# Optimization experiments

Hardware: AMD Instinct MI355X
Metric: run time of the kernel (lower is better)

Reference implementation:

```python
import jax, jax.numpy as jnp
import numpy as np

# ---- constants mirroring tinyRSNN __init__ ----
DT = 0.004
THRESHOLD = 1.0
SOFTPLUS_1 = float(np.log1p(np.e))  # softplus(1.0) = 1.3132617
TAU_SYN_H = SOFTPLUS_1 * 0.01
TAU_MEM_H = SOFTPLUS_1 * 0.02
TAU_SYN_O = SOFTPLUS_1 * 0.01
TAU_MEM_O = SOFTPLUS_1 * 0.02

T, B, IN, H, OUT = 4096, 128, 96, 64, 2


def setup_inputs() -> dict:
    key = jax.random.key(0)
    k0, k1, k2, k3 = jax.random.split(key, 4)
    x = jax.random.normal(k0, (T, B, IN), dtype=jnp.float32)
    W_h = jax.random.normal(k1, (H, IN), dtype=jnp.float32) / np.sqrt(IN)
    V = jax.random.normal(k2, (H, H), dtype=jnp.float32) / np.sqrt(H)
    W_o = jax.random.normal(k3, (OUT, H), dtype=jnp.float32) / np.sqrt(H)
    return {"x": x, "W_h": W_h, "V": V, "W_o": W_o}


def _spike(u):
    # forward: Heaviside(u); surrogate gradient handled in fwdbwd module
    return (u > 0).astype(u.dtype)


def reference(x, W_h, V, W_o):
    # exponential decay factors (stork-like synaptic/membrane dynamics)
    alpha_h = jnp.exp(-DT / TAU_SYN_H)
    beta_h = jnp.exp(-DT / TAU_MEM_H)
    alpha_o = jnp.exp(-DT / TAU_SYN_O)
    beta_o = jnp.exp(-DT / TAU_MEM_O)

    def step(carry, x_t):
        prev_inp, spk, syn, mem, syn_o, mem_o = carry
        # NOTE: module feeds the PREVIOUS input and PREVIOUS hidden spikes
        cur_h = prev_inp @ W_h.T                       # [B,H]
        syn = alpha_h * syn + cur_h + spk @ V.T        # synaptic current
        mem = beta_h * mem + (1.0 - beta_h) * syn      # membrane integration
        new_spk = _spike(mem - THRESHOLD)              # threshold at 1
        mem = mem * (1.0 - new_spk)                    # reset_mechanism='zero'
        # readout LIF (reset_mechanism='none'), driven by previous spikes
        syn_o = alpha_o * syn_o + spk @ W_o.T
        mem_o = beta_o * mem_o + (1.0 - beta_o) * syn_o
        return (x_t, new_spk, syn, mem, syn_o, mem_o), mem_o

    z = lambda *s: jnp.zeros(s, dtype=x.dtype)
    init = (z(B, IN), z(B, H), z(B, H), z(B, H), z(B, OUT), z(B, OUT))
    _, preds = jax.lax.scan(step, init, x)             # preds: [T,B,OUT]
    return preds
```

## Files before the change

### kernel.cpp

```cpp
#include <hip/hip_runtime.h>
#include <cmath>

#define T_STEPS 4096
#define BATCH   128
#define NIN     96
#define NH      64

typedef unsigned short u16;

__device__ __forceinline__ float bf2f(u16 u) {
    unsigned v = ((unsigned)u) << 16;
    return __builtin_bit_cast(float, v);
}
__device__ __forceinline__ double d_alpha() { return exp(-0.004 / (log1p(exp(1.0)) * 0.01)); }
__device__ __forceinline__ double d_beta()  { return exp(-0.004 / (log1p(exp(1.0)) * 0.02)); }

__device__ __forceinline__ int sniff_part(const void* p, int nscan, int tid, int nthr) {
    const u16* q = (const u16*)p;
    int cnt = 0;
    for (int i = tid; i < nscan; i += nthr) {
        float v = bf2f(q[i]);
        if (!(fabsf(v) < 1e4f)) cnt++;
    }
    return cnt;
}
__device__ __forceinline__ int wave_sum(int c) {
#pragma unroll
    for (int d = 32; d >= 1; d >>= 1) c += __shfl_xor(c, d, 64);
    return c;
}

__device__ __forceinline__ void acc_chunk(float* __restrict__ acc,
                                          const float* __restrict__ xr,
                                          const float* __restrict__ wbase) {
#pragma unroll
    for (int h = 0; h < 64; ++h) {
        const float4* wr = (const float4*)(wbase + h * NIN);
        const float4 w0 = wr[0], w1 = wr[1], w2 = wr[2], w3 = wr[3];
        float c = acc[h];
        c = fmaf(xr[0],  w0.x, c); c = fmaf(xr[1],  w0.y, c);
        c = fmaf(xr[2],  w0.z, c); c = fmaf(xr[3],  w0.w, c);
        c = fmaf(xr[4],  w1.x, c); c = fmaf(xr[5],  w1.y, c);
        c = fmaf(xr[6],  w1.z, c); c = fmaf(xr[7],  w1.w, c);
        c = fmaf(xr[8],  w2.x, c); c = fmaf(xr[9],  w2.y, c);
        c = fmaf(xr[10], w2.z, c); c = fmaf(xr[11], w2.w, c);
        c = fmaf(xr[12], w3.x, c); c = fmaf(xr[13], w3.y, c);
        c = fmaf(xr[14], w3.z, c); c = fmaf(xr[15], w3.w, c);
        acc[h] = c;
    }
}

__global__ __launch_bounds__(256) void k_cur(const void* __restrict__ xv,
                                             const void* __restrict__ whv,
                                             float* __restrict__ cur) {
    const int NROWC = (T_STEPS - 1) * BATCH;
    const int tid = threadIdx.x;
    __shared__ int s_cnt[2];
    __shared__ __align__(16) float whs[NH * NIN];
    if (tid < 2) s_cnt[tid] = 0;
    __syncthreads();
    int c0 = sniff_part(xv, 512, tid, 256);
    int c1 = sniff_part(whv, 512, tid, 256);
    if (c0) atomicAdd(&s_cnt[0], c0);
    if (c1) atomicAdd(&s_cnt[1], c1);
    __syncthreads();
    const bool fx = s_cnt[0] >= 32, fw = s_cnt[1] >= 32;

    if (fw) {
        const float* w = (const float*)whv;
        for (int s = tid; s < NH * NIN; s += 256) whs[s] = w[s];
    } else {
        const u16* w = (const u16*)whv;
        for (int s = tid; s < NH * NIN; s += 256) whs[s] = bf2f(w[s]);
    }
    __syncthreads();

    const long r = (long)blockIdx.x * 256 + tid;
    if (r >= NROWC) {
        const long z = r - NROWC;
        if (z < BATCH) {
            float4 zero = {0.f, 0.f, 0.f, 0.f};
            float4* zp = (float4*)(cur + z * NH);
#pragma unroll
            for (int j = 0; j < 16; ++j) zp[j] = zero;
        }
        return;
    }

    float acc[64];
#pragma unroll
    for (int h = 0; h < 64; ++h) acc[h] = 0.f;

    if (!fx) {
        const uint4* xq = (const uint4*)((const u16*)xv + (size_t)r * NIN);
        uint4 n0 = xq[0], n1 = xq[1];
#pragma unroll 1
        for (int kb = 0; kb < 6; ++kb) {
            const uint4 a = n0, b = n1;
            if (kb < 5) { n0 = xq[(kb + 1) * 2]; n1 = xq[(kb + 1) * 2 + 1]; }
            const unsigned ua[8] = {a.x, a.y, a.z, a.w, b.x, b.y, b.z, b.w};
            float xr[16];
#pragma unroll
            for (int j = 0; j < 8; ++j) {
                xr[2 * j]     = bf2f((u16)(ua[j] & 0xFFFFu));
                xr[2 * j + 1] = bf2f((u16)(ua[j] >> 16));
            }
            acc_chunk(acc, xr, whs + kb * 16);
        }
    } else {
        const float4* xq = (const float4*)((const float*)xv + (size_t)r * NIN);
        float4 n0 = xq[0], n1 = xq[1], n2 = xq[2], n3 = xq[3];
#pragma unroll 1
        for (int kb = 0; kb < 6; ++kb) {
            const float4 a0 = n0, a1 = n1, a2 = n2, a3 = n3;
            if (kb < 5) {
                n0 = xq[(kb + 1) * 4];     n1 = xq[(kb + 1) * 4 + 1];
                n2 = xq[(kb + 1) * 4 + 2]; n3 = xq[(kb + 1) * 4 + 3];
            }
            const float xr[16] = {a0.x, a0.y, a0.z, a0.w, a1.x, a1.y, a1.z, a1.w,
                                  a2.x, a2.y, a2.z, a2.w, a3.x, a3.y, a3.z, a3.w};
            acc_chunk(acc, xr, whs + kb * 16);
        }
    }

    float4* op = (float4*)(cur + ((size_t)r + BATCH) * NH);
#pragma unroll
    for (int j = 0; j < 16; ++j) {
        float4 v;
        v.x = acc[4 * j]; v.y = acc[4 * j + 1]; v.z = acc[4 * j + 2]; v.w = acc[4 * j + 3];
        op[j] = v;
    }
}

__global__ __launch_bounds__(64, 1) void k_scan(const float* __restrict__ cur,
                                                const void* __restrict__ vv,
                                                _Float16* __restrict__ ftr) {
    const int b = blockIdx.x, h = threadIdx.x;
    const double alpha = d_alpha(), beta = d_beta(), ombeta = 1.0 - beta;
    const float alphaf = (float)alpha, betaf = (float)beta, ombetaf = (float)ombeta;

    const bool fv = wave_sum(sniff_part(vv, 512, h, 64)) >= 32;

    __shared__ float vlds[65 * NH];
    if (fv) {
        const float* vp = (const float*)vv;
        for (int s = h; s < NH * NH; s += 64) vlds[((s & 63) << 6) | (s >> 6)] = vp[s];
    } else {
        const u16* vp = (const u16*)vv;
        for (int s = h; s < NH * NH; s += 64) vlds[((s & 63) << 6) | (s >> 6)] = bf2f(vp[s]);
    }
    vlds[(64 << 6) | h] = 0.0f;
    __syncthreads();

    double syn = 0.0, mem = 0.0;
    float e = 0.f, f = 0.f, spkf = 0.f;

    const size_t STEP = (size_t)BATCH * NH;
    const float* cp = cur + (size_t)b * NH + h;
    _Float16* fp = ftr + (size_t)b * NH + h;

    float cbuf[8];
#pragma unroll
    for (int j = 0; j < 8; ++j) cbuf[j] = cp[(size_t)j * STEP];

    float r0 = 0.f, r1 = 0.f;
    unsigned long long mt = 0ull;
    double p = ombeta * fma(alpha, syn, (double)cbuf[0]);
    double q = 1.0 - beta * mem;

    for (int tt = 0; tt < T_STEPS; tt += 8) {
#pragma unroll
        for (int j = 0; j < 8; ++j) {
            const int t = tt + j;
            const float c = cbuf[j];
            cbuf[j] = cp[(size_t)(t + 8) * STEP];

            double rec = (double)r0 + (double)r1;
            while (mt) {
                const int k = (int)__builtin_ctzll(mt);
                mt &= mt - 1;
                rec += (double)vlds[(k << 6) | h];
            }

            const bool s = fma(ombeta, rec, p) > q;
            const unsigned long long mask = __ballot(s);

            {
                unsigned long long m = mask;
                const int k0 = m ? (int)__builtin_ctzll(m) : 64;
                m = m ? (m & (m - 1)) : 0ull;
                const int k1 = m ? (int)__builtin_ctzll(m) : 64;
                mt = m ? (m & (m - 1)) : 0ull;
                r0 = vlds[(k0 << 6) | h];
                r1 = vlds[(k1 << 6) | h];
            }
            __builtin_amdgcn_sched_barrier(0);

            syn = alpha * syn + ((double)c + rec);
            mem = beta * mem + ombeta * syn;

            e = fmaf(alphaf, e, spkf);
            f = fmaf(betaf, f, ombetaf * e);
            fp[(size_t)t * STEP] = (_Float16)f;

            mem = s ? 0.0 : mem;
            spkf = s ? 1.0f : 0.0f;

            const float cn = cbuf[(j + 1) & 7];
            p = ombeta * fma(alpha, syn, (double)cn);
            q = 1.0 - beta * mem;
        }
    }
}

__global__ __launch_bounds__(256) void k_out(const _Float16* __restrict__ ftr,
                                             const void* __restrict__ wov,
                                             float* __restrict__ out) {
    const int tid = threadIdx.x;
    __shared__ unsigned tile[256 * 34];
    __shared__ float wo[2][64];
    const bool fo = sniff_part(wov, 120, 0, 1) >= 7;
    if (fo) {
        if (tid < 128) wo[tid >> 6][tid & 63] = ((const float*)wov)[tid];
    } else {
        if (tid < 128) wo[tid >> 6][tid & 63] = bf2f(((const u16*)wov)[tid]);
    }

    const unsigned* src = (const unsigned*)(ftr + (size_t)blockIdx.x * 256 * NH);
#pragma unroll
    for (int i = 0; i < 32; ++i) {
        const int s = i * 256 + tid;
        tile[(s >> 5) * 34 + (s & 31)] = src[s];
    }
    __syncthreads();

    const size_t idx = (size_t)blockIdx.x * 256 + tid;
    const unsigned* up = &tile[tid * 34];
    float d0 = 0.f, d1 = 0.f;
#pragma unroll
    for (int j = 0; j < 32; ++j) {
        const unsigned u = up[j];
        const float f0 = (float)__builtin_bit_cast(_Float16, (unsigned short)(u & 0xFFFFu));
        const float f1 = (float)__builtin_bit_cast(_Float16, (unsigned short)(u >> 16));
        d0 = fmaf(f0, wo[0][2 * j], d0);
        d1 = fmaf(f0, wo[1][2 * j], d1);
        d0 = fmaf(f1, wo[0][2 * j + 1], d0);
        d1 = fmaf(f1, wo[1][2 * j + 1], d1);
    }
    float2 r; r.x = d0; r.y = d1;
    ((float2*)out)[idx] = r;
}

__global__ __launch_bounds__(64) void k_fused(const void* __restrict__ xv,
                                              const void* __restrict__ whv,
                                              const void* __restrict__ vv,
                                              const void* __restrict__ wov,
                                              float* __restrict__ out) {
    const int b = blockIdx.x, h = threadIdx.x;
    const double alpha = d_alpha(), beta = d_beta(), ombeta = 1.0 - beta;

    const bool fx = wave_sum(sniff_part(xv, 512, h, 64)) >= 32;
    const bool fw = wave_sum(sniff_part(whv, 512, h, 64)) >= 32;
    const bool fv = wave_sum(sniff_part(vv, 512, h, 64)) >= 32;
    const bool fo = wave_sum(sniff_part(wov, 120, h, 64)) >= 7;

    __shared__ float vlds[NH * NH];
    __shared__ float whl[NIN * NH];
    if (fv) { const float* vp = (const float*)vv;
        for (int s = h; s < NH * NH; s += 64) vlds[((s & 63) << 6) | (s >> 6)] = vp[s]; }
    else    { const u16* vp = (const u16*)vv;
        for (int s = h; s < NH * NH; s += 64) vlds[((s & 63) << 6) | (s >> 6)] = bf2f(vp[s]); }
    if (fw) { const float* wp = (const float*)whv;
        for (int s = h; s < NH * NIN; s += 64) whl[(s % 96) * 64 + (s / 96)] = wp[s]; }
    else    { const u16* wp = (const u16*)whv;
        for (int s = h; s < NH * NIN; s += 64) whl[(s % 96) * 64 + (s / 96)] = bf2f(wp[s]); }
    __syncthreads();

    double wo0, wo1;
    if (fo) { wo0 = (double)((const float*)wov)[h]; wo1 = (double)((const float*)wov)[64 + h]; }
    else    { wo0 = (double)bf2f(((const u16*)wov)[h]); wo1 = (double)bf2f(((const u16*)wov)[64 + h]); }

    double syn = 0.0, mem = 0.0, syno0 = 0.0, memo0 = 0.0, syno1 = 0.0, memo1 = 0.0;
    double spkd = 0.0;
    unsigned long long mask = 0ull;

    for (int t = 0; t < T_STEPS; ++t) {
        float c = 0.0f;
        if (t > 0) {
            const size_t off = ((size_t)(t - 1) * BATCH + b) * NIN;
            if (fx) { const float* xp = (const float*)xv + off;
                for (int i = 0; i < NIN; ++i) c = fmaf(xp[i], whl[i * 64 + h], c); }
            else    { const u16* xp = (const u16*)xv + off;
                for (int i = 0; i < NIN; ++i) c = fmaf(bf2f(xp[i]), whl[i * 64 + h], c); }
        }
        double rec = 0.0;
        unsigned long long m = mask;
        while (m) { const int k = __builtin_ctzll(m); m &= m - 1; rec += (double)vlds[(k << 6) | h]; }

        syn = alpha * syn + ((double)c + rec);
        mem = beta * mem + ombeta * syn;

        double p0 = spkd * wo0, p1 = spkd * wo1;
#pragma unroll
        for (int d = 32; d >= 1; d >>= 1) { p0 += __shfl_xor(p0, d, 64); p1 += __shfl_xor(p1, d, 64); }
        syno0 = alpha * syno0 + p0;
        memo0 = beta * memo0 + ombeta * syno0;
        syno1 = alpha * syno1 + p1;
        memo1 = beta * memo1 + ombeta * syno1;
        if (h == 0) {
            const size_t w = ((size_t)t * BATCH + b) * 2;
            out[w] = (float)memo0;
            out[w + 1] = (float)memo1;
        }

        const bool s = mem > 1.0;
        mem = s ? 0.0 : mem;
        spkd = s ? 1.0 : 0.0;
        mask = __ballot(s);
    }
}

extern "C" void kernel_launch(void* const* d_in, const int* in_sizes, int n_in,
                              void* d_out, int out_size, void* d_ws, size_t ws_size,
                              hipStream_t stream) {
    (void)in_sizes; (void)out_size;
    if (n_in < 4) return;
    const void* x  = d_in[0];
    const void* Wh = d_in[1];
    const void* V  = d_in[2];
    const void* Wo = d_in[3];
    float* out = (float*)d_out;

    const size_t NROW = (size_t)T_STEPS * BATCH;
    const size_t curB = NROW * NH * sizeof(float);
    const size_t ftrB = NROW * NH * sizeof(_Float16);

    if (ws_size >= curB + ftrB) {
        float* cur = (float*)d_ws;
        _Float16* ftr = (_Float16*)((char*)d_ws + curB);
        const int NBLK = (int)(NROW / 256);
        k_cur<<<NBLK, 256, 0, stream>>>(x, Wh, cur);
        k_scan<<<BATCH, 64, 0, stream>>>(cur, V, ftr);
        k_out<<<NROW / 256, 256, 0, stream>>>(ftr, Wo, out);
    } else {
        k_fused<<<BATCH, 64, 0, stream>>>(x, Wh, V, Wo, out);
    }
}
```

Before: 924.5 us.

## Retile input projection kernel as 4x16 register tiles with transposed LDS weights

The input-projection kernel now gives each thread 4 rows × 16 hidden units instead of 1 row × 64 units. Weights are stored transposed in LDS so the 16 consecutive h values can be read as float4s at each k. This is meant to reuse every loaded weight across 4 rows and every x value across 16 outputs, cutting LDS reads per FMA. It also makes all lanes of a wave read the same weights (broadcast). The cost is that each thread's x loads now stride across 4 rows, and k_cur is likely a small share of total time next to the sequential scan kernel.

```diff
diff --git a/kernel.cpp b/kernel.cpp
--- a/kernel.cpp
+++ b/kernel.cpp
@@ -30,33 +30,15 @@
     return c;
 }
 
-__device__ __forceinline__ void acc_chunk(float* __restrict__ acc,
-                                          const float* __restrict__ xr,
-                                          const float* __restrict__ wbase) {
-#pragma unroll
-    for (int h = 0; h < 64; ++h) {
-        const float4* wr = (const float4*)(wbase + h * NIN);
-        const float4 w0 = wr[0], w1 = wr[1], w2 = wr[2], w3 = wr[3];
-        float c = acc[h];
-        c = fmaf(xr[0],  w0.x, c); c = fmaf(xr[1],  w0.y, c);
-        c = fmaf(xr[2],  w0.z, c); c = fmaf(xr[3],  w0.w, c);
-        c = fmaf(xr[4],  w1.x, c); c = fmaf(xr[5],  w1.y, c);
-        c = fmaf(xr[6],  w1.z, c); c = fmaf(xr[7],  w1.w, c);
-        c = fmaf(xr[8],  w2.x, c); c = fmaf(xr[9],  w2.y, c);
-        c = fmaf(xr[10], w2.z, c); c = fmaf(xr[11], w2.w, c);
-        c = fmaf(xr[12], w3.x, c); c = fmaf(xr[13], w3.y, c);
-        c = fmaf(xr[14], w3.z, c); c = fmaf(xr[15], w3.w, c);
-        acc[h] = c;
-    }
-}
-
 __global__ __launch_bounds__(256) void k_cur(const void* __restrict__ xv,
                                              const void* __restrict__ whv,
                                              float* __restrict__ cur) {
     const int NROWC = (T_STEPS - 1) * BATCH;
     const int tid = threadIdx.x;
+    const int lane = tid & 63;
+    const int hg = tid >> 6;
     __shared__ int s_cnt[2];
-    __shared__ __align__(16) float whs[NH * NIN];
+    __shared__ __align__(16) float wt[NIN][NH];
     if (tid < 2) s_cnt[tid] = 0;
     __syncthreads();
     int c0 = sniff_part(xv, 512, tid, 256);
@@ -68,67 +50,131 @@
 
     if (fw) {
         const float* w = (const float*)whv;
-        for (int s = tid; s < NH * NIN; s += 256) whs[s] = w[s];
+        for (int s = tid; s < NH * NIN; s += 256) wt[s % NIN][s / NIN] = w[s];
     } else {
         const u16* w = (const u16*)whv;
-        for (int s = tid; s < NH * NIN; s += 256) whs[s] = bf2f(w[s]);
-    }
-    __syncthreads();
-
-    const long r = (long)blockIdx.x * 256 + tid;
-    if (r >= NROWC) {
-        const long z = r - NROWC;
-        if (z < BATCH) {
-            float4 zero = {0.f, 0.f, 0.f, 0.f};
-            float4* zp = (float4*)(cur + z * NH);
-#pragma unroll
-            for (int j = 0; j < 16; ++j) zp[j] = zero;
-        }
-        return;
-    }
-
-    float acc[64];
-#pragma unroll
-    for (int h = 0; h < 64; ++h) acc[h] = 0.f;
+        for (int s = tid; s < NH * NIN; s += 256) wt[s % NIN][s / NIN] = bf2f(w[s]);
+    }
+    __syncthreads();
+
+    const long rbase = (long)blockIdx.x * 256;
+    long rr[4];
+    bool val[4];
+#pragma unroll
+    for (int i = 0; i < 4; ++i) {
+        rr[i] = rbase + lane + 64 * i;
+        val[i] = rr[i] < NROWC;
+    }
+
+    float acc[4][16];
+#pragma unroll
+    for (int i = 0; i < 4; ++i)
+#pragma unroll
+        for (int j = 0; j < 16; ++j) acc[i][j] = 0.f;
+
+    const float* wbase = &wt[0][hg * 16];
 
     if (!fx) {
-        const uint4* xq = (const uint4*)((const u16*)xv + (size_t)r * NIN);
-        uint4 n0 = xq[0], n1 = xq[1];
+        const u16* xb = (const u16*)xv;
+        const uint4* xq[4];
+#pragma unroll
+        for (int i = 0; i < 4; ++i)
+            xq[i] = (const uint4*)(xb + (val[i] ? (size_t)rr[i] : 0) * NIN);
+        uint4 n0 = xq[0][0], n1 = xq[1][0], n2 = xq[2][0], n3 = xq[3][0];
 #pragma unroll 1
-        for (int kb = 0; kb < 6; ++kb) {
-            const uint4 a = n0, b = n1;
-            if (kb < 5) { n0 = xq[(kb + 1) * 2]; n1 = xq[(kb + 1) * 2 + 1]; }
-            const unsigned ua[8] = {a.x, a.y, a.z, a.w, b.x, b.y, b.z, b.w};
-            float xr[16];
-#pragma unroll
-            for (int j = 0; j < 8; ++j) {
-                xr[2 * j]     = bf2f((u16)(ua[j] & 0xFFFFu));
-                xr[2 * j + 1] = bf2f((u16)(ua[j] >> 16));
-            }
-            acc_chunk(acc, xr, whs + kb * 16);
-        }
-    } else {
-        const float4* xq = (const float4*)((const float*)xv + (size_t)r * NIN);
-        float4 n0 = xq[0], n1 = xq[1], n2 = xq[2], n3 = xq[3];
+        for (int kb = 0; kb < 12; ++kb) {
+            const uint4 a0 = n0, a1 = n1, a2 = n2, a3 = n3;
+            if (kb < 11) {
+                n0 = xq[0][kb + 1]; n1 = xq[1][kb + 1];
+                n2 = xq[2][kb + 1]; n3 = xq[3][kb + 1];
+            }
+            float xr[4][8];
+            const unsigned ua[4][4] = {{a0.x, a0.y, a0.z, a0.w}, {a1.x, a1.y, a1.z, a1.w},
+                                       {a2.x, a2.y, a2.z, a2.w}, {a3.x, a3.y, a3.z, a3.w}};
+#pragma unroll
+            for (int i = 0; i < 4; ++i)
+#pragma unroll
+                for (int j = 0; j < 4; ++j) {
+                    xr[i][2 * j]     = bf2f((u16)(ua[i][j] & 0xFFFFu));
+                    xr[i][2 * j + 1] = bf2f((u16)(ua[i][j] >> 16));
+                }
+#pragma unroll
+            for (int kk = 0; kk < 8; ++kk) {
+                const float4* wr = (const float4*)(wbase + (size_t)(kb * 8 + kk) * NH);
+                const float4 w0 = wr[0], w1 = wr[1], w2 = wr[2], w3 = wr[3];
+                const float wv[16] = {w0.x, w0.y, w0.z, w0.w, w1.x, w1.y, w1.z, w1.w,
+                                      w2.x, w2.y, w2.z, w2.w, w3.x, w3.y, w3.z, w3.w};
+#pragma unroll
+                for (int i = 0; i < 4; ++i) {
+                    const float xv_ = xr[i][kk];
+#pragma unroll
+                    for (int j = 0; j < 16; ++j) acc[i][j] = fmaf(xv_, wv[j], acc[i][j]);
+                }
+            }
+        }
+    } else {
+        const float* xb = (const float*)xv;
+        const float4* xq[4];
+#pragma unroll
+        for (int i = 0; i < 4; ++i)
+            xq[i] = (const float4*)(xb + (val[i] ? (size_t)rr[i] : 0) * NIN);
+        float4 p0[4], p1[4];
+#pragma unroll
+        for (int i = 0; i < 4; ++i) { p0[i] = xq[i][0]; p1[i] = xq[i][1]; }
 #pragma unroll 1
-        for (int kb = 0; kb < 6; ++kb) {
-            const float4 a0 = n0, a1 = n1, a2 = n2, a3 = n3;
-            if (kb < 5) {
-                n0 = xq[(kb + 1) * 4];     n1 = xq[(kb + 1) * 4 + 1];
-                n2 = xq[(kb + 1) * 4 + 2]; n3 = xq[(kb + 1) * 4 + 3];
-            }
-            const float xr[16] = {a0.x, a0.y, a0.z, a0.w, a1.x, a1.y, a1.z, a1.w,
-                                  a2.x, a2.y, a2.z, a2.w, a3.x, a3.y, a3.z, a3.w};
-            acc_chunk(acc, xr, whs + kb * 16);
-        }
-    }
-
-    float4* op = (float4*)(cur + ((size_t)r + BATCH) * NH);
-#pragma unroll
-    for (int j = 0; j < 16; ++j) {
-        float4 v;
-        v.x = acc[4 * j]; v.y = acc[4 * j + 1]; v.z = acc[4 * j + 2]; v.w = acc[4 * j + 3];
-        op[j] = v;
+        for (int kb = 0; kb < 12; ++kb) {
+            float4 a0[4], a1[4];
+#pragma unroll
+            for (int i = 0; i < 4; ++i) { a0[i] = p0[i]; a1[i] = p1[i]; }
+            if (kb < 11) {
+#pragma unroll
+                for (int i = 0; i < 4; ++i) {
+                    p0[i] = xq[i][(kb + 1) * 2];
+                    p1[i] = xq[i][(kb + 1) * 2 + 1];
+                }
+            }
+            float xr[4][8];
+#pragma unroll
+            for (int i = 0; i < 4; ++i) {
+                xr[i][0] = a0[i].x; xr[i][1] = a0[i].y; xr[i][2] = a0[i].z; xr[i][3] = a0[i].w;
+                xr[i][4] = a1[i].x; xr[i][5] = a1[i].y; xr[i][6] = a1[i].z; xr[i][7] = a1[i].w;
+            }
+#pragma unroll
+            for (int kk = 0; kk < 8; ++kk) {
+                const float4* wr = (const float4*)(wbase + (size_t)(kb * 8 + kk) * NH);
+                const float4 w0 = wr[0], w1 = wr[1], w2 = wr[2], w3 = wr[3];
+                const float wv[16] = {w0.x, w0.y, w0.z, w0.w, w1.x, w1.y, w1.z, w1.w,
+                                      w2.x, w2.y, w2.z, w2.w, w3.x, w3.y, w3.z, w3.w};
+#pragma unroll
+                for (int i = 0; i < 4; ++i) {
+                    const float xv_ = xr[i][kk];
+#pragma unroll
+                    for (int j = 0; j < 16; ++j) acc[i][j] = fmaf(xv_, wv[j], acc[i][j]);
+                }
+            }
+        }
+    }
+
+#pragma unroll
+    for (int i = 0; i < 4; ++i) {
+        if (val[i]) {
+            float4* op = (float4*)(cur + (size_t)(rr[i] + BATCH) * NH + hg * 16);
+#pragma unroll
+            for (int j = 0; j < 4; ++j) {
+                float4 v;
+                v.x = acc[i][4 * j]; v.y = acc[i][4 * j + 1];
+                v.z = acc[i][4 * j + 2]; v.w = acc[i][4 * j + 3];
+                op[j] = v;
+            }
+        } else {
+            const long z = rr[i] - NROWC;
+            if (z < BATCH) {
+                const float4 zero = {0.f, 0.f, 0.f, 0.f};
+                float4* zp = (float4*)(cur + (size_t)z * NH + hg * 16);
+#pragma unroll
+                for (int j = 0; j < 4; ++j) zp[j] = zero;
+            }
+        }
     }
 }
 
```

Result: slower. 961.3 us (+4.0%).
